# Optimization experiments

Measured on AMD Instinct MI355X. Metric: run time of the kernel, lower is better.

Reference implementation:

```python
import jax, jax.numpy as jnp
import numpy as np

D_MODEL = 64

def setup_inputs() -> dict:
    key = jax.random.key(0)
    ks = jax.random.split(key, 7)
    d = D_MODEL
    x = jax.random.normal(ks[0], (8, 4096, d), dtype=jnp.float32)
    # Linear weights stored torch-style [out, in]; init ~ U(-1/sqrt(d), 1/sqrt(d))
    lim = 1.0 / np.sqrt(d)
    def lin(k):
        kw, kb = jax.random.split(k)
        W = jax.random.uniform(kw, (d, d), minval=-lim, maxval=lim, dtype=jnp.float32)
        b = jax.random.uniform(kb, (d,), minval=-lim, maxval=lim, dtype=jnp.float32)
        return W, b
    Wq, bq = lin(ks[1])
    Wk, bk = lin(ks[2])
    Wv, bv = lin(ks[3])
    return {"x": x, "Wq": Wq, "bq": bq, "Wk": Wk, "bk": bk, "Wv": Wv, "bv": bv}

def reference(x, Wq, bq, Wk, bk, Wv, bv):
    # Linear projections (torch Linear: x @ W.T + b)
    Q = jnp.einsum('bsd,ed->bse', x, Wq) + bq
    K = jnp.einsum('bsd,ed->bse', x, Wk) + bk
    V = jnp.einsum('bsd,ed->bse', x, Wv) + bv
    scale = jnp.sqrt(jnp.asarray(x.shape[-1], dtype=jnp.float32))
    # The block loops in the source compute ALL blocks, so math == dense attention.
    scores = jnp.einsum('bqd,bkd->bqk', Q, K) / scale  # [B, S, S]
    attn = jax.nn.softmax(scores, axis=-1)
    out = jnp.einsum('bqk,bkd->bqd', attn, V)
    return out
```

## Files before the change

kernel.cpp:

```cpp
#include <hip/hip_runtime.h>
#include <stdint.h>


#define B_ 8
#define S_ 4096
#define D_ 64
#define THR 7.0f

typedef short bf16x8 __attribute__((ext_vector_type(8)));
typedef float f32x4 __attribute__((ext_vector_type(4)));

#define MFMA16(a, b, c) __builtin_amdgcn_mfma_f32_16x16x32_bf16((a), (b), (c), 0, 0, 0)

static __device__ __forceinline__ unsigned short f2bf(float x) {
  union { float f; unsigned u; } v; v.f = x;
  unsigned r = v.u + 0x7FFFu + ((v.u >> 16) & 1u);
  return (unsigned short)(r >> 16);
}
static __device__ __forceinline__ void gload16(const void* g, void* l) {
  __builtin_amdgcn_global_load_lds(
      (const __attribute__((address_space(1))) unsigned int*)g,
      (__attribute__((address_space(3))) unsigned int*)l, 16, 0, 0);
}

union U8 { unsigned short s[8]; uint4 v; };
union PB { int w[4]; bf16x8 v; };

__global__ __launch_bounds__(256) void proj_kernel(
    const float* __restrict__ x,
    const float* __restrict__ Wq, const float* __restrict__ bq,
    const float* __restrict__ Wk, const float* __restrict__ bk,
    const float* __restrict__ Wv, const float* __restrict__ bv,
    unsigned short* __restrict__ Qb, unsigned short* __restrict__ Kb,
    unsigned short* __restrict__ Vt) {
  __shared__ unsigned short xb[64 * 64];
  __shared__ unsigned short wb[3][64 * 64];
  __shared__ unsigned short vtmp[64 * 64];

  const int tid = threadIdx.x;
  const int blk = blockIdx.x;
  const int batch = blk >> 6;
  const int s0 = (blk & 63) << 6;

  const int row = tid >> 2, c0 = (tid & 3) << 4;
  const int sw = (row & 7) << 4;

  {
    const float* src = x + ((size_t)(batch * S_ + s0 + row)) * D_ + c0;
    U8 a, b;
#pragma unroll
    for (int i = 0; i < 8; i++) a.s[i] = f2bf(src[i]);
#pragma unroll
    for (int i = 0; i < 8; i++) b.s[i] = f2bf(src[8 + i]);
    char* lp = (char*)xb + row * 128;
    *(uint4*)(lp + ((c0 * 2) ^ sw)) = a.v;
    *(uint4*)(lp + ((c0 * 2 + 16) ^ sw)) = b.v;
  }
  {
    const float* Ws[3] = {Wq, Wk, Wv};
#pragma unroll
    for (int m = 0; m < 3; m++) {
      const float* src = Ws[m] + row * 64 + c0;
      U8 a, b;
#pragma unroll
      for (int i = 0; i < 8; i++) a.s[i] = f2bf(src[i]);
#pragma unroll
      for (int i = 0; i < 8; i++) b.s[i] = f2bf(src[8 + i]);
      char* lp = (char*)wb[m] + row * 128;
      *(uint4*)(lp + ((c0 * 2) ^ sw)) = a.v;
      *(uint4*)(lp + ((c0 * 2 + 16) ^ sw)) = b.v;
    }
  }
  __syncthreads();

  const int lane = tid & 63;
  const int w = tid >> 6;
  const int g = lane >> 4;
  const int lr = lane & 15;

  bf16x8 xa0, xa1;
  {
    const int xr = w * 16 + lr;
    const int swz = (xr & 7) << 4;
    const char* lp = (const char*)xb + xr * 128;
    xa0 = *(const bf16x8*)(lp + ((g * 16) ^ swz));
    xa1 = *(const bf16x8*)(lp + ((64 + g * 16) ^ swz));
  }

  f32x4 acc[3][4];
#pragma unroll
  for (int m = 0; m < 3; m++)
#pragma unroll
    for (int n = 0; n < 4; n++) { acc[m][n][0] = 0.f; acc[m][n][1] = 0.f; acc[m][n][2] = 0.f; acc[m][n][3] = 0.f; }
#pragma unroll
  for (int m = 0; m < 3; m++) {
#pragma unroll
    for (int n = 0; n < 4; n++) {
      const int erow = n * 16 + lr;
      const int swz = (erow & 7) << 4;
      const char* lp = (const char*)wb[m] + erow * 128;
      bf16x8 w0 = *(const bf16x8*)(lp + ((g * 16) ^ swz));
      bf16x8 w1 = *(const bf16x8*)(lp + ((64 + g * 16) ^ swz));
      acc[m][n] = MFMA16(xa0, w0, acc[m][n]);
      acc[m][n] = MFMA16(xa1, w1, acc[m][n]);
    }
  }
  __syncthreads();

  {
#pragma unroll
    for (int n = 0; n < 4; n++) {
      const float bq_ = bq[n * 16 + lr];
      const float bk_ = bk[n * 16 + lr];
      const float bv_ = bv[n * 16 + lr];
#pragma unroll
      for (int r = 0; r < 4; r++) {
        const int orow = w * 16 + 4 * g + r;
        const int cb = ((n * 16 + lr) * 2) ^ ((orow & 7) << 4);
        *(unsigned short*)((char*)xb + orow * 128 + cb) =
            f2bf((acc[0][n][r] + bq_) * 0.18033688011112042f);
        *(unsigned short*)((char*)wb[0] + orow * 128 + cb) = f2bf(acc[1][n][r] + bk_);
        vtmp[orow * 64 + n * 16 + lr] = f2bf(acc[2][n][r] + bv_);
      }
    }
  }
  __syncthreads();

  {
    const char* qs_ = (const char*)xb + row * 128;
    uint4 q0 = *(const uint4*)(qs_ + ((c0 * 2) ^ sw));
    uint4 q1 = *(const uint4*)(qs_ + ((c0 * 2 + 16) ^ sw));
    unsigned short* qd = Qb + ((size_t)batch * S_ + s0 + row) * D_ + c0;
    *(uint4*)qd = q0;
    *(uint4*)(qd + 8) = q1;

    const char* ks_ = (const char*)wb[0] + row * 128;
    uint4 k0 = *(const uint4*)(ks_ + ((c0 * 2) ^ sw));
    uint4 k1 = *(const uint4*)(ks_ + ((c0 * 2 + 16) ^ sw));
    unsigned short* kd = Kb + ((size_t)batch * S_ + s0 + row) * D_ + c0;
    *(uint4*)kd = k0;
    *(uint4*)(kd + 8) = k1;

    const int e = row, sc0 = c0;
    union { unsigned short s[16]; uint4 v[2]; } o;
#pragma unroll
    for (int i = 0; i < 16; i++) {
      const int sp = sc0 + i;
      const int u = sp & 31;
      const int kap = (sp & 32) + 16 * ((u >> 2) & 1) + 4 * (u >> 3) + (u & 3);
      o.s[i] = vtmp[kap * 64 + e];
    }
    uint4* dst = (uint4*)(Vt + (size_t)batch * (64 * S_) + (size_t)e * S_ + s0 + sc0);
    dst[0] = o.v[0];
    dst[1] = o.v[1];
  }
}

__global__ __launch_bounds__(256, 2) void attn_kernel(
    const unsigned short* __restrict__ Qb, const unsigned short* __restrict__ Kb,
    const unsigned short* __restrict__ Vt, float* __restrict__ out) {
  __shared__ char lds[65536];

  const int bid = blockIdx.x;
  const int batch = bid & 7;
  const int qblk = bid >> 3;
  const int tid = threadIdx.x;
  const int lane = tid & 63;
  const int w = tid >> 6;
  const int qh = w & 1;
  const int kh = w >> 1;
  const int lr = lane & 15;
  const int g = lane >> 4;
  const int swzR = (lr & 7) << 4;

  const size_t bOff = (size_t)batch * S_ * D_;

  bf16x8 qa[2][2];
  {
    const unsigned short* qbase = Qb + bOff + ((size_t)(qblk * 64 + qh * 32 + lr)) * D_;
    qa[0][0] = *(const bf16x8*)(qbase + g * 8);
    qa[0][1] = *(const bf16x8*)(qbase + 32 + g * 8);
    qa[1][0] = *(const bf16x8*)(qbase + 16 * D_ + g * 8);
    qa[1][1] = *(const bf16x8*)(qbase + 16 * D_ + 32 + g * 8);
  }

  f32x4 oacc[2][4];
#pragma unroll
  for (int qs = 0; qs < 2; qs++)
#pragma unroll
    for (int n = 0; n < 4; n++) { oacc[qs][n][0] = 0.f; oacc[qs][n][1] = 0.f; oacc[qs][n][2] = 0.f; oacc[qs][n][3] = 0.f; }
  float m_[2] = {-__builtin_inff(), -__builtin_inff()};
  float l_[2] = {0.f, 0.f};

  const int rsub = lane >> 3;
  const int csw = (((lane & 7) ^ rsub)) << 4;
  const char* KbaseB = (const char*)(Kb + bOff);
  const char* VbaseB = (const char*)(Vt + bOff);
  const int sh = w >> 1;
  const bool stK = ((w & 1) == 0);
  const char* ksrcBase = KbaseB + rsub * 128 + csw;
  const char* vsrcBase = VbaseB + rsub * 8192 + csw;
  char* const stagedst = lds + (sh << 14) + ((w & 1) << 13);

  auto STAGE = [&](int t, int buf) {
    const int kt = sh * 32 + t;
    char* ldst = stagedst + buf * 32768;
    if (stK) {
      const char* s0_ = ksrcBase + (size_t)kt * 8192;
#pragma unroll
      for (int c = 0; c < 8; c++) gload16(s0_ + c * 1024, ldst + c * 1024);
    } else {
      const char* s0_ = vsrcBase + (size_t)kt * 128;
#pragma unroll
      for (int c = 0; c < 8; c++) gload16(s0_ + c * 65536, ldst + c * 1024);
    }
  };

  f32x4 sacc[2][4];
  PB pb[2][2];

#define SOFTMAX_STEP()                                                                     \
  {                                                                                        \
    float lmax[2];                                                                         \
    _Pragma("unroll") for (int qs = 0; qs < 2; qs++) {                                     \
      float a0 = fmaxf(fmaxf(sacc[qs][0][0], sacc[qs][0][1]), fmaxf(sacc[qs][0][2], sacc[qs][0][3])); \
      float a1 = fmaxf(fmaxf(sacc[qs][1][0], sacc[qs][1][1]), fmaxf(sacc[qs][1][2], sacc[qs][1][3])); \
      float a2 = fmaxf(fmaxf(sacc[qs][2][0], sacc[qs][2][1]), fmaxf(sacc[qs][2][2], sacc[qs][2][3])); \
      float a3 = fmaxf(fmaxf(sacc[qs][3][0], sacc[qs][3][1]), fmaxf(sacc[qs][3][2], sacc[qs][3][3])); \
      lmax[qs] = fmaxf(fmaxf(a0, a1), fmaxf(a2, a3));                                      \
    }                                                                                      \
    const bool ok = (lmax[0] <= m_[0] + THR) && (lmax[1] <= m_[1] + THR);                  \
    if (!__all(ok)) {                                                                      \
      _Pragma("unroll") for (int qs = 0; qs < 2; qs++) {                                   \
        float mx = fmaxf(lmax[qs], __shfl_xor(lmax[qs], 16));                              \
        mx = fmaxf(mx, __shfl_xor(mx, 32));                                                \
        const float mn = fmaxf(m_[qs], mx);                                                \
        const float fac = __builtin_amdgcn_exp2f(m_[qs] - mn);                             \
        m_[qs] = mn;                                                                       \
        l_[qs] *= fac;                                                                     \
        _Pragma("unroll") for (int n = 0; n < 4; n++) oacc[qs][n] *= fac;                  \
      }                                                                                    \
    }                                                                                      \
    _Pragma("unroll") for (int qs = 0; qs < 2; qs++) {                                     \
      float p[16];                                                                         \
      _Pragma("unroll") for (int mm = 0; mm < 4; mm++)                                     \
        _Pragma("unroll") for (int r = 0; r < 4; r++)                                      \
          p[mm * 4 + r] = __builtin_amdgcn_exp2f(sacc[qs][mm][r] - m_[qs]);                \
      float u0 = (p[0] + p[1]) + (p[2] + p[3]);                                            \
      float u1 = (p[4] + p[5]) + (p[6] + p[7]);                                            \
      float u2 = (p[8] + p[9]) + (p[10] + p[11]);                                          \
      float u3 = (p[12] + p[13]) + (p[14] + p[15]);                                        \
      l_[qs] += (u0 + u1) + (u2 + u3);                                                     \
      _Pragma("unroll") for (int i = 0; i < 8; i++) {                                      \
        int r_;                                                                            \
        asm("v_cvt_pk_bf16_f32 %0, %1, %2" : "=v"(r_) : "v"(p[2 * i]), "v"(p[2 * i + 1])); \
        pb[qs][i >> 2].w[i & 3] = r_;                                                      \
      }                                                                                    \
    }                                                                                      \
  }

  STAGE(0, 0);
  __syncthreads();

  for (int t = 0; t < 32; t++) {
    const int buf = t & 1;
    if (t < 31) STAGE(t + 1, buf ^ 1);

    const char* Kl = lds + buf * 32768 + (kh << 14);
    const char* Vl = Kl + 8192;

    __builtin_amdgcn_s_setprio(1);
#pragma unroll
    for (int m = 0; m < 4; m++) {
      const char* kp = Kl + (m * 16 + lr) * 128;
      bf16x8 ka0 = *(const bf16x8*)(kp + ((g * 16) ^ swzR));
      bf16x8 ka1 = *(const bf16x8*)(kp + ((64 + g * 16) ^ swzR));
#pragma unroll
      for (int qs = 0; qs < 2; qs++) {
        f32x4 c; c[0] = 0.f; c[1] = 0.f; c[2] = 0.f; c[3] = 0.f;
        c = MFMA16(ka0, qa[qs][0], c);
        c = MFMA16(ka1, qa[qs][1], c);
        sacc[qs][m] = c;
      }
    }
    __builtin_amdgcn_s_setprio(0);

    SOFTMAX_STEP();

    __builtin_amdgcn_s_setprio(1);
#pragma unroll
    for (int n = 0; n < 4; n++) {
      const char* vp = Vl + (n * 16 + lr) * 128;
      bf16x8 va0 = *(const bf16x8*)(vp + ((g * 16) ^ swzR));
      bf16x8 va1 = *(const bf16x8*)(vp + ((64 + g * 16) ^ swzR));
#pragma unroll
      for (int qs = 0; qs < 2; qs++) {
        oacc[qs][n] = MFMA16(va0, pb[qs][0].v, oacc[qs][n]);
        oacc[qs][n] = MFMA16(va1, pb[qs][1].v, oacc[qs][n]);
      }
    }
    __builtin_amdgcn_s_setprio(0);
    __syncthreads();
  }

#pragma unroll
  for (int qs = 0; qs < 2; qs++) {
    l_[qs] += __shfl_xor(l_[qs], 16);
    l_[qs] += __shfl_xor(l_[qs], 32);
  }

  char* mbase = lds + (qh << 14);
  if (kh == 1) {
#pragma unroll
    for (int qs = 0; qs < 2; qs++) {
      const int q = qs * 16 + lr;
      char* rowp = mbase + q * 256;
#pragma unroll
      for (int n = 0; n < 4; n++)
        *(f32x4*)(rowp + ((n * 64 + g * 16) ^ ((lr & 7) << 4))) = oacc[qs][n];
    }
    if (g == 0) {
#pragma unroll
      for (int qs = 0; qs < 2; qs++) {
        float2 ml; ml.x = m_[qs]; ml.y = l_[qs];
        *(float2*)(mbase + 8192 + qs * 128 + lr * 8) = ml;
      }
    }
  }
  __syncthreads();
  if (kh == 0) {
#pragma unroll
    for (int qs = 0; qs < 2; qs++) {
      const float2 ml2 = *(const float2*)(mbase + 8192 + qs * 128 + lr * 8);
      const float mn = fmaxf(m_[qs], ml2.x);
      const float a1 = __builtin_amdgcn_exp2f(m_[qs] - mn);
      const float a2 = __builtin_amdgcn_exp2f(ml2.x - mn);
      const float inv = 1.0f / (l_[qs] * a1 + ml2.y * a2);
      const int q = qs * 16 + lr;
      const char* rowp = mbase + q * 256;
      float* orow = out + ((size_t)batch * S_ + qblk * 64 + qh * 32 + q) * D_;
#pragma unroll
      for (int n = 0; n < 4; n++) {
        f32x4 o2 = *(const f32x4*)(rowp + ((n * 64 + g * 16) ^ ((lr & 7) << 4)));
        f32x4 res = (oacc[qs][n] * a1 + o2 * a2) * inv;
        *(f32x4*)(orow + n * 16 + g * 4) = res;
      }
    }
  }
}

extern "C" void kernel_launch(void* const* d_in, const int* in_sizes, int n_in,
                              void* d_out, int out_size, void* d_ws, size_t ws_size,
                              hipStream_t stream) {
  const float* x  = (const float*)d_in[0];
  const float* Wq = (const float*)d_in[1];
  const float* bq = (const float*)d_in[2];
  const float* Wk = (const float*)d_in[3];
  const float* bk = (const float*)d_in[4];
  const float* Wv = (const float*)d_in[5];
  const float* bv = (const float*)d_in[6];

  unsigned short* Qb = (unsigned short*)d_ws;
  unsigned short* Kb = Qb + (size_t)B_ * S_ * D_;
  unsigned short* Vt = Kb + (size_t)B_ * S_ * D_;

  proj_kernel<<<512, 256, 0, stream>>>(x, Wq, bq, Wk, bk, Wv, bv, Qb, Kb, Vt);
  attn_kernel<<<512, 256, 0, stream>>>(Qb, Kb, Vt, (float*)d_out);
}
```

Measured before the change: 125.1 us.

## Restructure attention to per-wave KV split with 32x32 MFMA and four-way merge

The attention kernel now gives each of the four waves its own quarter of the key sequence, with private LDS staging. This removes the per-tile block-wide __syncthreads and the shared double buffer. It switches from 16x16x32 to 32x32x16 bf16 MFMA, so each wave handles all 64 queries as two 32-row blocks, and it merges four partial softmax states at the end instead of two. The projection kernel vectorizes its fp32 loads with float4 and simplifies the V-transpose index math. The per-wave staging relies on explicit waitcnt with a single buffer per wave, so load latency may be less hidden, and the larger accumulators raise register pressure.

```diff
diff --git a/kernel.cpp b/kernel.cpp
--- a/kernel.cpp
+++ b/kernel.cpp
@@ -9,8 +9,10 @@
 
 typedef short bf16x8 __attribute__((ext_vector_type(8)));
 typedef float f32x4 __attribute__((ext_vector_type(4)));
+typedef float f32x16 __attribute__((ext_vector_type(16)));
 
 #define MFMA16(a, b, c) __builtin_amdgcn_mfma_f32_16x16x32_bf16((a), (b), (c), 0, 0, 0)
+#define MFMA32(a, b, c) __builtin_amdgcn_mfma_f32_32x32x16_bf16((a), (b), (c), 0, 0, 0)
 
 static __device__ __forceinline__ unsigned short f2bf(float x) {
   union { float f; unsigned u; } v; v.f = x;
@@ -46,12 +48,16 @@
   const int sw = (row & 7) << 4;
 
   {
-    const float* src = x + ((size_t)(batch * S_ + s0 + row)) * D_ + c0;
+    const float4* src = (const float4*)(x + ((size_t)(batch * S_ + s0 + row)) * D_ + c0);
+    float4 f[4];
+#pragma unroll
+    for (int i = 0; i < 4; i++) f[i] = src[i];
+    const float* ff = (const float*)f;
     U8 a, b;
 #pragma unroll
-    for (int i = 0; i < 8; i++) a.s[i] = f2bf(src[i]);
-#pragma unroll
-    for (int i = 0; i < 8; i++) b.s[i] = f2bf(src[8 + i]);
+    for (int i = 0; i < 8; i++) a.s[i] = f2bf(ff[i]);
+#pragma unroll
+    for (int i = 0; i < 8; i++) b.s[i] = f2bf(ff[8 + i]);
     char* lp = (char*)xb + row * 128;
     *(uint4*)(lp + ((c0 * 2) ^ sw)) = a.v;
     *(uint4*)(lp + ((c0 * 2 + 16) ^ sw)) = b.v;
@@ -60,12 +66,16 @@
     const float* Ws[3] = {Wq, Wk, Wv};
 #pragma unroll
     for (int m = 0; m < 3; m++) {
-      const float* src = Ws[m] + row * 64 + c0;
+      const float4* src = (const float4*)(Ws[m] + row * 64 + c0);
+      float4 f[4];
+#pragma unroll
+      for (int i = 0; i < 4; i++) f[i] = src[i];
+      const float* ff = (const float*)f;
       U8 a, b;
 #pragma unroll
-      for (int i = 0; i < 8; i++) a.s[i] = f2bf(src[i]);
-#pragma unroll
-      for (int i = 0; i < 8; i++) b.s[i] = f2bf(src[8 + i]);
+      for (int i = 0; i < 8; i++) a.s[i] = f2bf(ff[i]);
+#pragma unroll
+      for (int i = 0; i < 8; i++) b.s[i] = f2bf(ff[8 + i]);
       char* lp = (char*)wb[m] + row * 128;
       *(uint4*)(lp + ((c0 * 2) ^ sw)) = a.v;
       *(uint4*)(lp + ((c0 * 2 + 16) ^ sw)) = b.v;
@@ -145,9 +155,7 @@
     union { unsigned short s[16]; uint4 v[2]; } o;
 #pragma unroll
     for (int i = 0; i < 16; i++) {
-      const int sp = sc0 + i;
-      const int u = sp & 31;
-      const int kap = (sp & 32) + 16 * ((u >> 2) & 1) + 4 * (u >> 3) + (u & 3);
+      const int kap = sc0 + ((i & 3) | ((i & 4) << 1) | ((i & 8) >> 1));
       o.s[i] = vtmp[kap * 64 + e];
     }
     uint4* dst = (uint4*)(Vt + (size_t)batch * (64 * S_) + (size_t)e * S_ + s0 + sc0);
@@ -167,185 +175,194 @@
   const int tid = threadIdx.x;
   const int lane = tid & 63;
   const int w = tid >> 6;
-  const int qh = w & 1;
-  const int kh = w >> 1;
-  const int lr = lane & 15;
-  const int g = lane >> 4;
-  const int swzR = (lr & 7) << 4;
+  const int q32 = lane & 31;
+  const int hi = lane >> 5;
+  const int swz = (q32 & 7) << 4;
 
   const size_t bOff = (size_t)batch * S_ * D_;
-
-  bf16x8 qa[2][2];
-  {
-    const unsigned short* qbase = Qb + bOff + ((size_t)(qblk * 64 + qh * 32 + lr)) * D_;
-    qa[0][0] = *(const bf16x8*)(qbase + g * 8);
-    qa[0][1] = *(const bf16x8*)(qbase + 32 + g * 8);
-    qa[1][0] = *(const bf16x8*)(qbase + 16 * D_ + g * 8);
-    qa[1][1] = *(const bf16x8*)(qbase + 16 * D_ + 32 + g * 8);
-  }
-
-  f32x4 oacc[2][4];
-#pragma unroll
-  for (int qs = 0; qs < 2; qs++)
-#pragma unroll
-    for (int n = 0; n < 4; n++) { oacc[qs][n][0] = 0.f; oacc[qs][n][1] = 0.f; oacc[qs][n][2] = 0.f; oacc[qs][n][3] = 0.f; }
+  char* const wbase = lds + (w << 14);
+
+  bf16x8 qa[2][4];
+#pragma unroll
+  for (int qb = 0; qb < 2; qb++) {
+    const unsigned short* qp = Qb + bOff + (size_t)(qblk * 64 + qb * 32 + q32) * D_ + hi * 8;
+#pragma unroll
+    for (int c = 0; c < 4; c++) qa[qb][c] = *(const bf16x8*)(qp + c * 16);
+  }
+
+  f32x16 oacc[2][2];
+#pragma unroll
+  for (int qb = 0; qb < 2; qb++)
+#pragma unroll
+    for (int n = 0; n < 2; n++)
+#pragma unroll
+      for (int i = 0; i < 16; i++) oacc[qb][n][i] = 0.f;
   float m_[2] = {-__builtin_inff(), -__builtin_inff()};
   float l_[2] = {0.f, 0.f};
 
   const int rsub = lane >> 3;
-  const int csw = (((lane & 7) ^ rsub)) << 4;
-  const char* KbaseB = (const char*)(Kb + bOff);
-  const char* VbaseB = (const char*)(Vt + bOff);
-  const int sh = w >> 1;
-  const bool stK = ((w & 1) == 0);
-  const char* ksrcBase = KbaseB + rsub * 128 + csw;
-  const char* vsrcBase = VbaseB + rsub * 8192 + csw;
-  char* const stagedst = lds + (sh << 14) + ((w & 1) << 13);
-
-  auto STAGE = [&](int t, int buf) {
-    const int kt = sh * 32 + t;
-    char* ldst = stagedst + buf * 32768;
-    if (stK) {
-      const char* s0_ = ksrcBase + (size_t)kt * 8192;
-#pragma unroll
-      for (int c = 0; c < 8; c++) gload16(s0_ + c * 1024, ldst + c * 1024);
-    } else {
-      const char* s0_ = vsrcBase + (size_t)kt * 128;
-#pragma unroll
-      for (int c = 0; c < 8; c++) gload16(s0_ + c * 65536, ldst + c * 1024);
+  const int csw = ((lane & 7) ^ rsub) << 4;
+  const char* ksrc0 = (const char*)(Kb + bOff) + rsub * 128 + csw;
+  const char* vsrc0 = (const char*)(Vt + bOff) + rsub * 8192 + csw;
+  char* const kdst = wbase + lane * 16;
+  char* const vdst = wbase + 8192 + lane * 16;
+
+  auto STAGE = [&](int kt) {
+    const char* ks = ksrc0 + (size_t)kt * 8192;
+    const char* vs = vsrc0 + (size_t)kt * 128;
+#pragma unroll
+    for (int c = 0; c < 8; c++) {
+      gload16(ks + c * 1024, kdst + c * 1024);
+      gload16(vs + c * 65536, vdst + c * 1024);
     }
   };
 
-  f32x4 sacc[2][4];
-  PB pb[2][2];
-
-#define SOFTMAX_STEP()                                                                     \
-  {                                                                                        \
-    float lmax[2];                                                                         \
-    _Pragma("unroll") for (int qs = 0; qs < 2; qs++) {                                     \
-      float a0 = fmaxf(fmaxf(sacc[qs][0][0], sacc[qs][0][1]), fmaxf(sacc[qs][0][2], sacc[qs][0][3])); \
-      float a1 = fmaxf(fmaxf(sacc[qs][1][0], sacc[qs][1][1]), fmaxf(sacc[qs][1][2], sacc[qs][1][3])); \
-      float a2 = fmaxf(fmaxf(sacc[qs][2][0], sacc[qs][2][1]), fmaxf(sacc[qs][2][2], sacc[qs][2][3])); \
-      float a3 = fmaxf(fmaxf(sacc[qs][3][0], sacc[qs][3][1]), fmaxf(sacc[qs][3][2], sacc[qs][3][3])); \
-      lmax[qs] = fmaxf(fmaxf(a0, a1), fmaxf(a2, a3));                                      \
-    }                                                                                      \
-    const bool ok = (lmax[0] <= m_[0] + THR) && (lmax[1] <= m_[1] + THR);                  \
-    if (!__all(ok)) {                                                                      \
-      _Pragma("unroll") for (int qs = 0; qs < 2; qs++) {                                   \
-        float mx = fmaxf(lmax[qs], __shfl_xor(lmax[qs], 16));                              \
-        mx = fmaxf(mx, __shfl_xor(mx, 32));                                                \
-        const float mn = fmaxf(m_[qs], mx);                                                \
-        const float fac = __builtin_amdgcn_exp2f(m_[qs] - mn);                             \
-        m_[qs] = mn;                                                                       \
-        l_[qs] *= fac;                                                                     \
-        _Pragma("unroll") for (int n = 0; n < 4; n++) oacc[qs][n] *= fac;                  \
-      }                                                                                    \
-    }                                                                                      \
-    _Pragma("unroll") for (int qs = 0; qs < 2; qs++) {                                     \
-      float p[16];                                                                         \
-      _Pragma("unroll") for (int mm = 0; mm < 4; mm++)                                     \
-        _Pragma("unroll") for (int r = 0; r < 4; r++)                                      \
-          p[mm * 4 + r] = __builtin_amdgcn_exp2f(sacc[qs][mm][r] - m_[qs]);                \
-      float u0 = (p[0] + p[1]) + (p[2] + p[3]);                                            \
-      float u1 = (p[4] + p[5]) + (p[6] + p[7]);                                            \
-      float u2 = (p[8] + p[9]) + (p[10] + p[11]);                                          \
-      float u3 = (p[12] + p[13]) + (p[14] + p[15]);                                        \
-      l_[qs] += (u0 + u1) + (u2 + u3);                                                     \
-      _Pragma("unroll") for (int i = 0; i < 8; i++) {                                      \
-        int r_;                                                                            \
-        asm("v_cvt_pk_bf16_f32 %0, %1, %2" : "=v"(r_) : "v"(p[2 * i]), "v"(p[2 * i + 1])); \
-        pb[qs][i >> 2].w[i & 3] = r_;                                                      \
-      }                                                                                    \
-    }                                                                                      \
-  }
-
-  STAGE(0, 0);
+  STAGE(w * 16);
+
+  for (int t = 0; t < 16; t++) {
+    asm volatile("s_waitcnt vmcnt(0)" ::: "memory");
+
+    bf16x8 ka[2][4], va[2][4];
+#pragma unroll
+    for (int m = 0; m < 2; m++) {
+      const char* kp = wbase + (m * 32 + q32) * 128;
+#pragma unroll
+      for (int c = 0; c < 4; c++)
+        ka[m][c] = *(const bf16x8*)(kp + ((c * 32 + hi * 16) ^ swz));
+    }
+#pragma unroll
+    for (int n = 0; n < 2; n++) {
+      const char* vp = wbase + 8192 + (n * 32 + q32) * 128;
+#pragma unroll
+      for (int s = 0; s < 4; s++)
+        va[n][s] = *(const bf16x8*)(vp + ((s * 32 + hi * 16) ^ swz));
+    }
+
+    asm volatile("s_waitcnt lgkmcnt(0)" ::: "memory");
+    if (t < 15) STAGE(w * 16 + t + 1);
+
+#pragma unroll
+    for (int qb = 0; qb < 2; qb++) {
+      f32x16 sa[2];
+#pragma unroll
+      for (int m = 0; m < 2; m++) {
+#pragma unroll
+        for (int i = 0; i < 16; i++) sa[m][i] = 0.f;
+      }
+      __builtin_amdgcn_s_setprio(1);
+#pragma unroll
+      for (int m = 0; m < 2; m++)
+#pragma unroll
+        for (int c = 0; c < 4; c++) sa[m] = MFMA32(ka[m][c], qa[qb][c], sa[m]);
+      __builtin_amdgcn_s_setprio(0);
+
+      float tm[16];
+#pragma unroll
+      for (int i = 0; i < 16; i++) tm[i] = fmaxf(sa[0][i], sa[1][i]);
+#pragma unroll
+      for (int i = 0; i < 8; i++) tm[i] = fmaxf(tm[i], tm[i + 8]);
+#pragma unroll
+      for (int i = 0; i < 4; i++) tm[i] = fmaxf(tm[i], tm[i + 4]);
+      const float lmax = fmaxf(fmaxf(tm[0], tm[1]), fmaxf(tm[2], tm[3]));
+      if (!__all(lmax <= m_[qb] + THR)) {
+        const float mx = fmaxf(lmax, __shfl_xor(lmax, 32));
+        const float mn = fmaxf(m_[qb], mx);
+        const float fac = __builtin_amdgcn_exp2f(m_[qb] - mn);
+        m_[qb] = mn;
+        l_[qb] *= fac;
+        oacc[qb][0] *= fac;
+        oacc[qb][1] *= fac;
+      }
+#pragma unroll
+      for (int m = 0; m < 2; m++)
+#pragma unroll
+        for (int i = 0; i < 16; i++) sa[m][i] = __builtin_amdgcn_exp2f(sa[m][i] - m_[qb]);
+      float ts[16];
+#pragma unroll
+      for (int i = 0; i < 16; i++) ts[i] = sa[0][i] + sa[1][i];
+#pragma unroll
+      for (int i = 0; i < 8; i++) ts[i] += ts[i + 8];
+#pragma unroll
+      for (int i = 0; i < 4; i++) ts[i] += ts[i + 4];
+      l_[qb] += (ts[0] + ts[1]) + (ts[2] + ts[3]);
+
+      PB pbs[4];
+#pragma unroll
+      for (int s = 0; s < 4; s++) {
+        const int m = s >> 1, h = (s & 1) * 8;
+#pragma unroll
+        for (int i = 0; i < 4; i++) {
+          int r_;
+          asm("v_cvt_pk_bf16_f32 %0, %1, %2"
+              : "=v"(r_) : "v"(sa[m][h + 2 * i]), "v"(sa[m][h + 2 * i + 1]));
+          pbs[s].w[i] = r_;
+        }
+      }
+
+      __builtin_amdgcn_s_setprio(1);
+#pragma unroll
+      for (int n = 0; n < 2; n++)
+#pragma unroll
+        for (int s = 0; s < 4; s++) oacc[qb][n] = MFMA32(va[n][s], pbs[s].v, oacc[qb][n]);
+      __builtin_amdgcn_s_setprio(0);
+    }
+  }
+
+#pragma unroll
+  for (int qb = 0; qb < 2; qb++) l_[qb] += __shfl_xor(l_[qb], 32);
+
   __syncthreads();
 
-  for (int t = 0; t < 32; t++) {
-    const int buf = t & 1;
-    if (t < 31) STAGE(t + 1, buf ^ 1);
-
-    const char* Kl = lds + buf * 32768 + (kh << 14);
-    const char* Vl = Kl + 8192;
-
-    __builtin_amdgcn_s_setprio(1);
-#pragma unroll
-    for (int m = 0; m < 4; m++) {
-      const char* kp = Kl + (m * 16 + lr) * 128;
-      bf16x8 ka0 = *(const bf16x8*)(kp + ((g * 16) ^ swzR));
-      bf16x8 ka1 = *(const bf16x8*)(kp + ((64 + g * 16) ^ swzR));
-#pragma unroll
-      for (int qs = 0; qs < 2; qs++) {
-        f32x4 c; c[0] = 0.f; c[1] = 0.f; c[2] = 0.f; c[3] = 0.f;
-        c = MFMA16(ka0, qa[qs][0], c);
-        c = MFMA16(ka1, qa[qs][1], c);
-        sacc[qs][m] = c;
-      }
-    }
-    __builtin_amdgcn_s_setprio(0);
-
-    SOFTMAX_STEP();
-
-    __builtin_amdgcn_s_setprio(1);
-#pragma unroll
-    for (int n = 0; n < 4; n++) {
-      const char* vp = Vl + (n * 16 + lr) * 128;
-      bf16x8 va0 = *(const bf16x8*)(vp + ((g * 16) ^ swzR));
-      bf16x8 va1 = *(const bf16x8*)(vp + ((64 + g * 16) ^ swzR));
-#pragma unroll
-      for (int qs = 0; qs < 2; qs++) {
-        oacc[qs][n] = MFMA16(va0, pb[qs][0].v, oacc[qs][n]);
-        oacc[qs][n] = MFMA16(va1, pb[qs][1].v, oacc[qs][n]);
-      }
-    }
-    __builtin_amdgcn_s_setprio(0);
+#pragma unroll
+  for (int ph = 0; ph < 2; ph++) {
+    {
+      char* ob = lds + w * 8192 + q32 * 256;
+#pragma unroll
+      for (int n = 0; n < 2; n++)
+#pragma unroll
+        for (int u = 0; u < 4; u++) {
+          f32x4 vv;
+          vv[0] = oacc[ph][n][4 * u + 0];
+          vv[1] = oacc[ph][n][4 * u + 1];
+          vv[2] = oacc[ph][n][4 * u + 2];
+          vv[3] = oacc[ph][n][4 * u + 3];
+          const int chunk = 2 * u + hi + 8 * n;
+          *(f32x4*)(ob + ((chunk * 16) ^ swz)) = vv;
+        }
+      if (hi == 0) {
+        float2 ml; ml.x = m_[ph]; ml.y = l_[ph];
+        *(float2*)(lds + 32768 + w * 256 + q32 * 8) = ml;
+      }
+    }
     __syncthreads();
-  }
-
-#pragma unroll
-  for (int qs = 0; qs < 2; qs++) {
-    l_[qs] += __shfl_xor(l_[qs], 16);
-    l_[qs] += __shfl_xor(l_[qs], 32);
-  }
-
-  char* mbase = lds + (qh << 14);
-  if (kh == 1) {
-#pragma unroll
-    for (int qs = 0; qs < 2; qs++) {
-      const int q = qs * 16 + lr;
-      char* rowp = mbase + q * 256;
-#pragma unroll
-      for (int n = 0; n < 4; n++)
-        *(f32x4*)(rowp + ((n * 64 + g * 16) ^ ((lr & 7) << 4))) = oacc[qs][n];
-    }
-    if (g == 0) {
-#pragma unroll
-      for (int qs = 0; qs < 2; qs++) {
-        float2 ml; ml.x = m_[qs]; ml.y = l_[qs];
-        *(float2*)(mbase + 8192 + qs * 128 + lr * 8) = ml;
-      }
-    }
-  }
-  __syncthreads();
-  if (kh == 0) {
-#pragma unroll
-    for (int qs = 0; qs < 2; qs++) {
-      const float2 ml2 = *(const float2*)(mbase + 8192 + qs * 128 + lr * 8);
-      const float mn = fmaxf(m_[qs], ml2.x);
-      const float a1 = __builtin_amdgcn_exp2f(m_[qs] - mn);
-      const float a2 = __builtin_amdgcn_exp2f(ml2.x - mn);
-      const float inv = 1.0f / (l_[qs] * a1 + ml2.y * a2);
-      const int q = qs * 16 + lr;
-      const char* rowp = mbase + q * 256;
-      float* orow = out + ((size_t)batch * S_ + qblk * 64 + qh * 32 + q) * D_;
-#pragma unroll
-      for (int n = 0; n < 4; n++) {
-        f32x4 o2 = *(const f32x4*)(rowp + ((n * 64 + g * 16) ^ ((lr & 7) << 4)));
-        f32x4 res = (oacc[qs][n] * a1 + o2 * a2) * inv;
-        *(f32x4*)(orow + n * 16 + g * 4) = res;
-      }
-    }
+    {
+      const int q = w * 8 + (lane >> 3);
+      const int dc = (lane & 7) * 2;
+      const int qsw = (q & 7) << 4;
+      float2 ml[4];
+#pragma unroll
+      for (int w4 = 0; w4 < 4; w4++) ml[w4] = *(const float2*)(lds + 32768 + w4 * 256 + q * 8);
+      const float M = fmaxf(fmaxf(ml[0].x, ml[1].x), fmaxf(ml[2].x, ml[3].x));
+      float a[4], L = 0.f;
+#pragma unroll
+      for (int w4 = 0; w4 < 4; w4++) { a[w4] = __builtin_amdgcn_exp2f(ml[w4].x - M); L += a[w4] * ml[w4].y; }
+      f32x4 o0, o1;
+      o0[0] = o0[1] = o0[2] = o0[3] = 0.f;
+      o1[0] = o1[1] = o1[2] = o1[3] = 0.f;
+#pragma unroll
+      for (int w4 = 0; w4 < 4; w4++) {
+        const char* pb_ = lds + w4 * 8192 + q * 256;
+        f32x4 r0 = *(const f32x4*)(pb_ + ((dc * 16) ^ qsw));
+        f32x4 r1 = *(const f32x4*)(pb_ + (((dc + 1) * 16) ^ qsw));
+        o0 += r0 * a[w4];
+        o1 += r1 * a[w4];
+      }
+      const float inv = 1.0f / L;
+      float* orow = out + ((size_t)batch * S_ + qblk * 64 + ph * 32 + q) * D_ + (lane & 7) * 8;
+      *(f32x4*)orow = o0 * inv;
+      *(f32x4*)(orow + 4) = o1 * inv;
+    }
+    __syncthreads();
   }
 }
 
```

Measured after the change: 128.6 us. +2.8%, slower.
